# Performance work log

Measured on AMD Instinct MI355X. Metric: run time of the kernel, lower is better.

## Reference

```python
import jax, jax.numpy as jnp
import numpy as np

# --- fixed model configuration (from init_kwargs) ---
Nx, Nu, Ny, Np = 3, 1, 2, 5
Nz = Np * (Ny + Nu)          # 15
F, V, DELTA = 0.1, 1.0, 1.0  # ps (flow), volume, sampling time
CAMEAN, CBMEAN = 0.5, 0.4    # yscale means
CASTD, CBSTD = 0.3, 0.2      # yscale stds
CAFMEAN, CAFSTD = 1.0, 0.5   # uscale


def _fnn(x, W1, b1, W2, b2):
    # dense(tanh) -> dense(linear), as createDenseLayers/fnnTf
    return jnp.tanh(x @ W1 + b1) @ W2 + b2


def setup_inputs() -> dict:
    B, T = 4096, 1024
    key = jax.random.key(0)
    ks = jax.random.split(key, 16)
    g = lambda k, shp, fan: (jax.random.normal(k, shp, jnp.float32) / np.sqrt(fan))
    return {
        "u": jax.random.normal(ks[0], (B, T, Nu), jnp.float32),
        "xz0": jax.random.normal(ks[1], (B, Nx + Nz), jnp.float32),
        "r1_W1": g(ks[2], (1, 16), 1),  "r1_b1": jnp.zeros((16,), jnp.float32),
        "r1_W2": g(ks[3], (16, 1), 16), "r1_b2": jnp.zeros((1,), jnp.float32),
        "r2_W1": g(ks[4], (2, 16), 2),  "r2_b1": jnp.zeros((16,), jnp.float32),
        "r2_W2": g(ks[5], (16, 1), 16), "r2_b2": jnp.zeros((1,), jnp.float32),
        "eC_W1": g(ks[6], (Nz, 32), Nz), "eC_b1": jnp.zeros((32,), jnp.float32),
        "eC_W2": g(ks[7], (32, 1), 32),  "eC_b2": jnp.zeros((1,), jnp.float32),
    }


def _forward(u, xz0, r1_W1, r1_b1, r1_W2, r1_b2,
             r2_W1, r2_b1, r2_W2, r2_b2, eC_W1, eC_b1, eC_W2, eC_b2):

    def fxu(x, uu):
        Ca, Cb, Cc = x[:, 0:1], x[:, 1:2], x[:, 2:3]
        Caf = uu[:, 0:1]
        r1 = _fnn(Ca, r1_W1, r1_b1, r1_W2, r1_b2) * CASTD
        r2 = _fnn(jnp.concatenate((Cb, Cc), -1), r2_W1, r2_b1, r2_W2, r2_b2) * CBSTD
        Ca = Ca * CASTD + CAMEAN
        Cb = Cb * CBSTD + CBMEAN
        Cc = Cc * CBSTD + CBMEAN
        Caf = Caf * CAFSTD + CAFMEAN
        dCa = F * (Caf - Ca) / V - r1
        dCb = -F * Cb / V + r1 - 3.0 * r2
        dCc = -F * Cc / V + r2
        return jnp.concatenate([dCa / CASTD, dCb / CBSTD, dCc / CBSTD], -1)

    # initial state: replace Cc with NN estimate from past data z0
    y0 = xz0[:, :Ny]
    z0 = xz0[:, Nx:]
    Cc0 = _fnn(z0, eC_W1, eC_b1, eC_W2, eC_b2)
    xz = jnp.concatenate((y0, Cc0, z0), -1)  # [B, Nx+Nz]

    def step(xz, uu):
        x, z = xz[:, :Nx], xz[:, Nx:]
        ypseq, upseq = z[:, :Np * Ny], z[:, Np * Ny:]
        k1 = fxu(x, uu)
        k2 = fxu(x + DELTA * (k1 / 2.0), uu)
        k3 = fxu(x + DELTA * (k2 / 2.0), uu)
        k4 = fxu(x + DELTA * k3, uu)
        xplus = x + (DELTA / 6.0) * (k1 + 2.0 * k2 + 2.0 * k3 + k4)
        zplus = jnp.concatenate((ypseq[:, Ny:], x[:, :Ny], upseq[:, Nu:], uu), -1)
        CcNN = _fnn(z, eC_W1, eC_b1, eC_W2, eC_b2)
        y = jnp.concatenate((x, CcNN), -1)  # [B, Nx+1]
        return jnp.concatenate((xplus, zplus), -1), y

    u_t = jnp.swapaxes(u, 0, 1)  # [T, B, Nu]
    _, ys = jax.lax.scan(step, xz, u_t)
    yseq_full = jnp.swapaxes(ys, 0, 1)      # [B, T, Nx+1]
    yseq = yseq_full[..., :Ny]
    xseq = yseq_full[..., :Nx]
    return yseq_full, yseq, xseq


def reference(u, xz0, r1_W1, r1_b1, r1_W2, r1_b2,
              r2_W1, r2_b1, r2_W2, r2_b2, eC_W1, eC_b1, eC_W2, eC_b2):
    return _forward(u, xz0, r1_W1, r1_b1, r1_W2, r1_b2,
                    r2_W1, r2_b1, r2_W2, r2_b2, eC_W1, eC_b1, eC_W2, eC_b2)
```

## Files before the change

### kernel.cpp

```cpp
#include <hip/hip_runtime.h>
#include <stdint.h>
#include <math.h>

#define NB 4096
#define NT 1024


#if __has_builtin(__builtin_amdgcn_exp2f)
#define EXP2F __builtin_amdgcn_exp2f
#else
#define EXP2F exp2f
#endif
#if __has_builtin(__builtin_amdgcn_rcpf)
#define RCPF __builtin_amdgcn_rcpf
#else
#define RCPF(x) (1.0f / (x))
#endif

__device__ __forceinline__ float fast_tanh(float y) {
  float e = EXP2F(y * 2.885390081777927f);
  float r = RCPF(e + 1.0f);
  return __builtin_fmaf(-2.0f, r, 1.0f);
}

template <int CTRL>
__device__ __forceinline__ float dppmov(float x) {
  return __int_as_float(
      __builtin_amdgcn_update_dpp(0, __float_as_int(x), CTRL, 0xF, 0xF, true));
}

__device__ __forceinline__ void rowred2(float& a, float& b) {
  a += dppmov<0x128>(a); b += dppmov<0x128>(b);
  a += dppmov<0x124>(a); b += dppmov<0x124>(b);
  a += dppmov<0x122>(a); b += dppmov<0x122>(b);
  a += dppmov<0x121>(a); b += dppmov<0x121>(b);
}
__device__ __forceinline__ float rowred1(float a) {
  a += dppmov<0x128>(a);
  a += dppmov<0x124>(a);
  a += dppmov<0x122>(a);
  a += dppmov<0x121>(a);
  return a;
}

__global__ __launch_bounds__(256) void phase1_kernel(
    const float* __restrict__ u, const float* __restrict__ xz0,
    const float* __restrict__ r1W1, const float* __restrict__ r1b1,
    const float* __restrict__ r1W2, const float* __restrict__ r1b2,
    const float* __restrict__ r2W1, const float* __restrict__ r2b1,
    const float* __restrict__ r2W2, const float* __restrict__ r2b2,
    const float* __restrict__ eCW1, const float* __restrict__ eCb1,
    const float* __restrict__ eCW2, const float* __restrict__ eCb2,
    float* __restrict__ out) {
  const int lane = threadIdx.x & 15;
  const int chain = (blockIdx.x << 4) + (threadIdx.x >> 4);

  const float w1a = r1W1[lane];
  const float w1b = r1b1[lane];
  const float w1c = r1W2[lane];
  const float c1 = r1b2[0];
  const float w2a = r2W1[lane];
  const float w2b = r2W1[16 + lane];
  const float w2c = r2b1[lane];
  const float w2d = r2W2[lane];
  const float c2 = r2b2[0];

  const float* xzr = xz0 + chain * 18;
  float x0 = xzr[0];
  float x1 = xzr[1];

  float hA = eCb1[lane], hB = eCb1[lane + 16];
#pragma unroll
  for (int i = 0; i < 15; ++i) {
    const float z = xzr[3 + i];
    hA = __builtin_fmaf(z, eCW1[i * 32 + lane], hA);
    hB = __builtin_fmaf(z, eCW1[i * 32 + lane + 16], hB);
  }
  float p = fast_tanh(hA) * eCW2[lane] + fast_tanh(hB) * eCW2[lane + 16];
  float x2 = rowred1(p) + eCb2[0];

  const float* urow = u + (size_t)chain * NT;
  float* yf = out + (size_t)chain * NT * 4;
  float* ys = out + (size_t)NB * NT * 4 + (size_t)chain * NT * 2;
  float* xs = out + (size_t)NB * NT * 6 + (size_t)chain * NT * 3;

  float a_u;
  auto fxu = [&](float s0, float s1, float s2, float& k0, float& k1,
                 float& k2) {
    float p1 = fast_tanh(__builtin_fmaf(s0, w1a, w1b)) * w1c;
    float p2 =
        fast_tanh(__builtin_fmaf(s1, w2a, __builtin_fmaf(s2, w2b, w2c))) * w2d;
    rowred2(p1, p2);
    const float n1 = p1 + c1;
    const float n2 = p2 + c2;
    k0 = __builtin_fmaf(-0.1f, s0, a_u) - n1;
    float t1 = __builtin_fmaf(-0.1f, s1, -0.2f);
    t1 = __builtin_fmaf(1.5f, n1, t1);
    k1 = __builtin_fmaf(-3.0f, n2, t1);
    k2 = __builtin_fmaf(-0.1f, s2, -0.2f) + n2;
  };

  float4 ucur = *(const float4*)urow;
  for (int t4 = 0; t4 < NT; t4 += 4) {
    const int tn = (t4 + 4 < NT) ? (t4 + 4) : (NT - 4);
    const float4 unext = *(const float4*)(urow + tn);
    float us[4] = {ucur.x, ucur.y, ucur.z, ucur.w};
#pragma unroll
    for (int e = 0; e < 4; ++e) {
      const int t = t4 + e;
      if (lane == 0) {
        *(float2*)(yf + t * 4) = make_float2(x0, x1);
        yf[t * 4 + 2] = x2;
        *(float2*)(ys + t * 2) = make_float2(x0, x1);
        xs[t * 3 + 0] = x0;
        xs[t * 3 + 1] = x1;
        xs[t * 3 + 2] = x2;
      }
      const float uu = us[e];
      a_u = __builtin_fmaf(uu, 1.0f / 6.0f, 1.0f / 6.0f);
      float k10, k11, k12, k20, k21, k22, k30, k31, k32, k40, k41, k42;
      fxu(x0, x1, x2, k10, k11, k12);
      fxu(__builtin_fmaf(0.5f, k10, x0), __builtin_fmaf(0.5f, k11, x1),
          __builtin_fmaf(0.5f, k12, x2), k20, k21, k22);
      fxu(__builtin_fmaf(0.5f, k20, x0), __builtin_fmaf(0.5f, k21, x1),
          __builtin_fmaf(0.5f, k22, x2), k30, k31, k32);
      fxu(x0 + k30, x1 + k31, x2 + k32, k40, k41, k42);
      x0 += (k10 + 2.0f * (k20 + k30) + k40) * (1.0f / 6.0f);
      x1 += (k11 + 2.0f * (k21 + k31) + k41) * (1.0f / 6.0f);
      x2 += (k12 + 2.0f * (k22 + k32) + k42) * (1.0f / 6.0f);
    }
    ucur = unext;
  }
}

__global__ __launch_bounds__(256) void phase2_kernel(
    const float* __restrict__ u, const float* __restrict__ xz0,
    const float* __restrict__ eCW1, const float* __restrict__ eCb1,
    const float* __restrict__ eCW2, const float* __restrict__ eCb2,
    float* __restrict__ out) {
  __shared__ float lw[32][16];
  __shared__ float lw2[32];
  const int tid = threadIdx.x;
  if (tid < 32) {
#pragma unroll
    for (int i = 0; i < 15; ++i) lw[tid][i] = eCW1[i * 32 + tid];
    lw[tid][15] = eCb1[tid];
    lw2[tid] = eCW2[tid];
  }
  __syncthreads();

  const int b = blockIdx.x;
  const int t0 = tid << 2;
  const float2* ysrow =
      (const float2*)(out + (size_t)NB * NT * 4) + (size_t)b * NT;
  const float* urow = u + (size_t)b * NT;
  const float* xzr = xz0 + b * 18;

  float yw[16], uw[8];
#pragma unroll
  for (int idx = 0; idx < 8; ++idx) {
    const int tp = t0 - 5 + idx;
    float a, c, uu;
    if (tp >= 0) {
      const float2 h = ysrow[tp];
      a = h.x;
      c = h.y;
      uu = urow[tp];
    } else {
      a = xzr[3 + 2 * (tp + 5)];
      c = xzr[4 + 2 * (tp + 5)];
      uu = xzr[13 + (tp + 5)];
    }
    yw[2 * idx] = a;
    yw[2 * idx + 1] = c;
    uw[idx] = uu;
  }

  float acc[4] = {0.f, 0.f, 0.f, 0.f};
  for (int j = 0; j < 32; ++j) {
    const float4 wa = ((const float4*)lw[j])[0];
    const float4 wb = ((const float4*)lw[j])[1];
    const float4 wc = ((const float4*)lw[j])[2];
    const float4 wd = ((const float4*)lw[j])[3];
    const float w2 = lw2[j];
#pragma unroll
    for (int e = 0; e < 4; ++e) {
      float h = wd.w;
      h = __builtin_fmaf(yw[2 * e + 0], wa.x, h);
      h = __builtin_fmaf(yw[2 * e + 1], wa.y, h);
      h = __builtin_fmaf(yw[2 * e + 2], wa.z, h);
      h = __builtin_fmaf(yw[2 * e + 3], wa.w, h);
      h = __builtin_fmaf(yw[2 * e + 4], wb.x, h);
      h = __builtin_fmaf(yw[2 * e + 5], wb.y, h);
      h = __builtin_fmaf(yw[2 * e + 6], wb.z, h);
      h = __builtin_fmaf(yw[2 * e + 7], wb.w, h);
      h = __builtin_fmaf(yw[2 * e + 8], wc.x, h);
      h = __builtin_fmaf(yw[2 * e + 9], wc.y, h);
      h = __builtin_fmaf(uw[e + 0], wc.z, h);
      h = __builtin_fmaf(uw[e + 1], wc.w, h);
      h = __builtin_fmaf(uw[e + 2], wd.x, h);
      h = __builtin_fmaf(uw[e + 3], wd.y, h);
      h = __builtin_fmaf(uw[e + 4], wd.z, h);
      acc[e] = __builtin_fmaf(fast_tanh(h), w2, acc[e]);
    }
  }
  const float b2v = eCb2[0];
  float* yfrow = out + (size_t)b * NT * 4;
#pragma unroll
  for (int e = 0; e < 4; ++e) {
    yfrow[(t0 + e) * 4 + 3] = acc[e] + b2v;
  }
}

extern "C" void kernel_launch(void* const* d_in, const int* in_sizes, int n_in,
                              void* d_out, int out_size, void* d_ws,
                              size_t ws_size, hipStream_t stream) {
  const float* u = (const float*)d_in[0];
  const float* xz0 = (const float*)d_in[1];
  const float* r1W1 = (const float*)d_in[2];
  const float* r1b1 = (const float*)d_in[3];
  const float* r1W2 = (const float*)d_in[4];
  const float* r1b2 = (const float*)d_in[5];
  const float* r2W1 = (const float*)d_in[6];
  const float* r2b1 = (const float*)d_in[7];
  const float* r2W2 = (const float*)d_in[8];
  const float* r2b2 = (const float*)d_in[9];
  const float* eCW1 = (const float*)d_in[10];
  const float* eCb1 = (const float*)d_in[11];
  const float* eCW2 = (const float*)d_in[12];
  const float* eCb2 = (const float*)d_in[13];
  float* out = (float*)d_out;

  hipLaunchKernelGGL(phase1_kernel, dim3(NB / 16), dim3(256), 0, stream, u,
                     xz0, r1W1, r1b1, r1W2, r1b2, r2W1, r2b1, r2W2, r2b2, eCW1,
                     eCb1, eCW2, eCb2, out);
  hipLaunchKernelGGL(phase2_kernel, dim3(NB), dim3(256), 0, stream, u, xz0,
                     eCW1, eCb1, eCW2, eCb2, out);
}
```

Measured before the change: 680.6 us.

## Split RK4 state across two 16-lane DPP rows per chain and fold tanh constants

Phase 1 now gives each chain 32 lanes. One DPP row evaluates the r1 network and owns Ca, and the other row evaluates r2 and owns (Cb, Cc), so each lane computes a single tanh per RK stage instead of two. The r1 sum is broadcast across rows with a row_bcast DPP. The tanh scale and the -2*W2 factor are folded into the weights in both kernels, which removes multiplies from the inner loops. This doubles the thread count for phase 1 and lowers the work per lane on the serial recurrence, but it adds a cross-row DPP dependency and leaves more lanes idle during stores.

```diff
diff --git a/kernel.cpp b/kernel.cpp
--- a/kernel.cpp
+++ b/kernel.cpp
@@ -17,30 +17,29 @@
 #define RCPF(x) (1.0f / (x))
 #endif
 
-__device__ __forceinline__ float fast_tanh(float y) {
-  float e = EXP2F(y * 2.885390081777927f);
-  float r = RCPF(e + 1.0f);
-  return __builtin_fmaf(-2.0f, r, 1.0f);
-}
+#define TANH_SCALE 2.885390081777927f
 
 template <int CTRL>
 __device__ __forceinline__ float dppmov(float x) {
   return __int_as_float(
       __builtin_amdgcn_update_dpp(0, __float_as_int(x), CTRL, 0xF, 0xF, true));
 }
-
-__device__ __forceinline__ void rowred2(float& a, float& b) {
-  a += dppmov<0x128>(a); b += dppmov<0x128>(b);
-  a += dppmov<0x124>(a); b += dppmov<0x124>(b);
-  a += dppmov<0x122>(a); b += dppmov<0x122>(b);
-  a += dppmov<0x121>(a); b += dppmov<0x121>(b);
-}
+template <int CTRL, int RMASK>
+__device__ __forceinline__ float dppmov_keep(float x) {
+  return __int_as_float(__builtin_amdgcn_update_dpp(
+      __float_as_int(x), __float_as_int(x), CTRL, RMASK, 0xF, false));
+}
+
 __device__ __forceinline__ float rowred1(float a) {
   a += dppmov<0x128>(a);
   a += dppmov<0x124>(a);
   a += dppmov<0x122>(a);
   a += dppmov<0x121>(a);
   return a;
+}
+
+__device__ __forceinline__ float bcast_r1sum(float x) {
+  return dppmov_keep<0x142, 0xA>(x);
 }
 
 __global__ __launch_bounds__(256) void phase1_kernel(
@@ -52,82 +51,105 @@
     const float* __restrict__ eCW1, const float* __restrict__ eCb1,
     const float* __restrict__ eCW2, const float* __restrict__ eCb2,
     float* __restrict__ out) {
-  const int lane = threadIdx.x & 15;
-  const int chain = (blockIdx.x << 4) + (threadIdx.x >> 4);
-
-  const float w1a = r1W1[lane];
-  const float w1b = r1b1[lane];
-  const float w1c = r1W2[lane];
+  const int tid = threadIdx.x;
+  const int sub = tid & 31;
+  const int rl = tid & 15;
+  const bool row1 = (sub & 16) != 0;
+  const int chain = (blockIdx.x << 3) + (tid >> 5);
+
+  float wA, wB, wC, wP;
+  if (!row1) {
+    wA = r1W1[rl] * TANH_SCALE;
+    wB = 0.0f;
+    wC = r1b1[rl] * TANH_SCALE;
+    wP = r1W2[rl];
+  } else {
+    wA = r2W1[rl] * TANH_SCALE;
+    wB = r2W1[16 + rl] * TANH_SCALE;
+    wC = r2b1[rl] * TANH_SCALE;
+    wP = r2W2[rl];
+  }
+  const float wPn2 = -2.0f * wP;
   const float c1 = r1b2[0];
-  const float w2a = r2W1[lane];
-  const float w2b = r2W1[16 + lane];
-  const float w2c = r2b1[lane];
-  const float w2d = r2W2[lane];
   const float c2 = r2b2[0];
 
+  const float gA1 = row1 ? 1.5f : -1.0f;
+  const float gA2 = row1 ? -3.0f : 0.0f;
+  const float mB = row1 ? -0.1f : 0.0f;
+  const float cBc = row1 ? -0.2f : 0.0f;
+  const float gB2 = row1 ? 1.0f : 0.0f;
+  const float uCoef = row1 ? 0.0f : (1.0f / 6.0f);
+  const float uBias = row1 ? -0.2f : (1.0f / 6.0f);
+
   const float* xzr = xz0 + chain * 18;
-  float x0 = xzr[0];
-  float x1 = xzr[1];
-
-  float hA = eCb1[lane], hB = eCb1[lane + 16];
-#pragma unroll
-  for (int i = 0; i < 15; ++i) {
-    const float z = xzr[3 + i];
-    hA = __builtin_fmaf(z, eCW1[i * 32 + lane], hA);
-    hB = __builtin_fmaf(z, eCW1[i * 32 + lane + 16], hB);
-  }
-  float p = fast_tanh(hA) * eCW2[lane] + fast_tanh(hB) * eCW2[lane + 16];
-  float x2 = rowred1(p) + eCb2[0];
+  float xA = row1 ? xzr[1] : xzr[0];
+
+  float h0 = eCb1[sub];
+#pragma unroll
+  for (int i = 0; i < 15; ++i)
+    h0 = __builtin_fmaf(xzr[3 + i], eCW1[i * 32 + sub], h0);
+  const float e0 = EXP2F(h0 * TANH_SCALE);
+  const float r0 = RCPF(e0 + 1.0f);
+  float p0 = __builtin_fmaf(-2.0f * eCW2[sub], r0, eCW2[sub]);
+  p0 = rowred1(p0);
+  const float q0 = __int_as_float(
+      __builtin_amdgcn_ds_swizzle(__float_as_int(p0), 0x401F));
+  const float x2init = p0 + q0 + eCb2[0];
+  float xB = row1 ? x2init : 0.0f;
 
   const float* urow = u + (size_t)chain * NT;
-  float* yf = out + (size_t)chain * NT * 4;
-  float* ys = out + (size_t)NB * NT * 4 + (size_t)chain * NT * 2;
-  float* xs = out + (size_t)NB * NT * 6 + (size_t)chain * NT * 3;
-
-  float a_u;
-  auto fxu = [&](float s0, float s1, float s2, float& k0, float& k1,
-                 float& k2) {
-    float p1 = fast_tanh(__builtin_fmaf(s0, w1a, w1b)) * w1c;
-    float p2 =
-        fast_tanh(__builtin_fmaf(s1, w2a, __builtin_fmaf(s2, w2b, w2c))) * w2d;
-    rowred2(p1, p2);
-    const float n1 = p1 + c1;
-    const float n2 = p2 + c2;
-    k0 = __builtin_fmaf(-0.1f, s0, a_u) - n1;
-    float t1 = __builtin_fmaf(-0.1f, s1, -0.2f);
-    t1 = __builtin_fmaf(1.5f, n1, t1);
-    k1 = __builtin_fmaf(-3.0f, n2, t1);
-    k2 = __builtin_fmaf(-0.1f, s2, -0.2f) + n2;
+  const int ro = row1 ? 1 : 0;
+  float* yfb = out + (size_t)chain * NT * 4 + ro;
+  float* ysb = out + (size_t)NB * NT * 4 + (size_t)chain * NT * 2 + ro;
+  float* xsb = out + (size_t)NB * NT * 6 + (size_t)chain * NT * 3 + ro;
+
+  auto fxu = [&](float sA, float sB, float cA, float& kA, float& kB) {
+    float h = __builtin_fmaf(sB, wB, wC);
+    h = __builtin_fmaf(sA, wA, h);
+    const float e = EXP2F(h);
+    const float r = RCPF(e + 1.0f);
+    float p = __builtin_fmaf(wPn2, r, wP);
+    p = rowred1(p);
+    const float n1 = bcast_r1sum(p) + c1;
+    const float n2 = p + c2;
+    kA = __builtin_fmaf(-0.1f, sA, cA);
+    kA = __builtin_fmaf(gA1, n1, kA);
+    kA = __builtin_fmaf(gA2, n2, kA);
+    kB = __builtin_fmaf(mB, sB, cBc);
+    kB = __builtin_fmaf(gB2, n2, kB);
   };
 
   float4 ucur = *(const float4*)urow;
   for (int t4 = 0; t4 < NT; t4 += 4) {
     const int tn = (t4 + 4 < NT) ? (t4 + 4) : (NT - 4);
     const float4 unext = *(const float4*)(urow + tn);
-    float us[4] = {ucur.x, ucur.y, ucur.z, ucur.w};
+    const float us[4] = {ucur.x, ucur.y, ucur.z, ucur.w};
 #pragma unroll
     for (int e = 0; e < 4; ++e) {
       const int t = t4 + e;
-      if (lane == 0) {
-        *(float2*)(yf + t * 4) = make_float2(x0, x1);
-        yf[t * 4 + 2] = x2;
-        *(float2*)(ys + t * 2) = make_float2(x0, x1);
-        xs[t * 3 + 0] = x0;
-        xs[t * 3 + 1] = x1;
-        xs[t * 3 + 2] = x2;
+      if (rl == 0) {
+        yfb[t * 4] = xA;
+        ysb[t * 2] = xA;
+        xsb[t * 3] = xA;
       }
-      const float uu = us[e];
-      a_u = __builtin_fmaf(uu, 1.0f / 6.0f, 1.0f / 6.0f);
-      float k10, k11, k12, k20, k21, k22, k30, k31, k32, k40, k41, k42;
-      fxu(x0, x1, x2, k10, k11, k12);
-      fxu(__builtin_fmaf(0.5f, k10, x0), __builtin_fmaf(0.5f, k11, x1),
-          __builtin_fmaf(0.5f, k12, x2), k20, k21, k22);
-      fxu(__builtin_fmaf(0.5f, k20, x0), __builtin_fmaf(0.5f, k21, x1),
-          __builtin_fmaf(0.5f, k22, x2), k30, k31, k32);
-      fxu(x0 + k30, x1 + k31, x2 + k32, k40, k41, k42);
-      x0 += (k10 + 2.0f * (k20 + k30) + k40) * (1.0f / 6.0f);
-      x1 += (k11 + 2.0f * (k21 + k31) + k41) * (1.0f / 6.0f);
-      x2 += (k12 + 2.0f * (k22 + k32) + k42) * (1.0f / 6.0f);
+      if (sub == 16) {
+        yfb[t * 4 + 1] = xB;
+        xsb[t * 3 + 1] = xB;
+      }
+      const float cA = __builtin_fmaf(us[e], uCoef, uBias);
+      float k1A, k1B, k2A, k2B, k3A, k3B, k4A, k4B;
+      fxu(xA, xB, cA, k1A, k1B);
+      fxu(__builtin_fmaf(0.5f, k1A, xA), __builtin_fmaf(0.5f, k1B, xB), cA,
+          k2A, k2B);
+      fxu(__builtin_fmaf(0.5f, k2A, xA), __builtin_fmaf(0.5f, k2B, xB), cA,
+          k3A, k3B);
+      fxu(xA + k3A, xB + k3B, cA, k4A, k4B);
+      float tA = k2A + k3A;
+      tA = __builtin_fmaf(2.0f, tA, k1A) + k4A;
+      xA = __builtin_fmaf(1.0f / 6.0f, tA, xA);
+      float tB = k2B + k3B;
+      tB = __builtin_fmaf(2.0f, tB, k1B) + k4B;
+      xB = __builtin_fmaf(1.0f / 6.0f, tB, xB);
     }
     ucur = unext;
   }
@@ -143,9 +165,9 @@
   const int tid = threadIdx.x;
   if (tid < 32) {
 #pragma unroll
-    for (int i = 0; i < 15; ++i) lw[tid][i] = eCW1[i * 32 + tid];
-    lw[tid][15] = eCb1[tid];
-    lw2[tid] = eCW2[tid];
+    for (int i = 0; i < 15; ++i) lw[tid][i] = eCW1[i * 32 + tid] * TANH_SCALE;
+    lw[tid][15] = eCb1[tid] * TANH_SCALE;
+    lw2[tid] = -2.0f * eCW2[tid];
   }
   __syncthreads();
 
@@ -182,7 +204,7 @@
     const float4 wb = ((const float4*)lw[j])[1];
     const float4 wc = ((const float4*)lw[j])[2];
     const float4 wd = ((const float4*)lw[j])[3];
-    const float w2 = lw2[j];
+    const float w2n = lw2[j];
 #pragma unroll
     for (int e = 0; e < 4; ++e) {
       float h = wd.w;
@@ -201,14 +223,18 @@
       h = __builtin_fmaf(uw[e + 2], wd.x, h);
       h = __builtin_fmaf(uw[e + 3], wd.y, h);
       h = __builtin_fmaf(uw[e + 4], wd.z, h);
-      acc[e] = __builtin_fmaf(fast_tanh(h), w2, acc[e]);
+      const float r = RCPF(EXP2F(h) + 1.0f);
+      acc[e] = __builtin_fmaf(w2n, r, acc[e]);
     }
   }
-  const float b2v = eCb2[0];
+  float sw = 0.0f;
+#pragma unroll
+  for (int j = 0; j < 32; ++j) sw += eCW2[j];
+  const float C = eCb2[0] + sw;
   float* yfrow = out + (size_t)b * NT * 4;
 #pragma unroll
   for (int e = 0; e < 4; ++e) {
-    yfrow[(t0 + e) * 4 + 3] = acc[e] + b2v;
+    yfrow[(t0 + e) * 4 + 3] = acc[e] + C;
   }
 }
 
@@ -231,8 +257,8 @@
   const float* eCb2 = (const float*)d_in[13];
   float* out = (float*)d_out;
 
-  hipLaunchKernelGGL(phase1_kernel, dim3(NB / 16), dim3(256), 0, stream, u,
-                     xz0, r1W1, r1b1, r1W2, r1b2, r2W1, r2b1, r2W2, r2b2, eCW1,
+  hipLaunchKernelGGL(phase1_kernel, dim3(NB / 8), dim3(256), 0, stream, u, xz0,
+                     r1W1, r1b1, r1W2, r1b2, r2W1, r2b1, r2W2, r2b2, eCW1,
                      eCb1, eCW2, eCb2, out);
   hipLaunchKernelGGL(phase2_kernel, dim3(NB), dim3(256), 0, stream, u, xz0,
                      eCW1, eCb1, eCW2, eCb2, out);
```

Measured after the change: 682.8 us. No clear change (+0.3%).

## Fuse Cc estimator into recurrence kernel and spread output stores across lanes

Applied to the files above, without the earlier changes.

Merges the two-kernel approach into one kernel: the eC network for each timestep is computed inline within the 16-lane group, using a sliding register window of past y and u instead of a second kernel that re-reads the stored y sequence. Output writes are spread across lanes (each lane owns one output column) rather than funnelled through lane 0. Tanh scaling constants and biases are folded into the weights so each activation needs fewer ops. Blocks shrink to 64 threads. This adds about 32 extra FMAs plus 2 exp/rcp and one reduction per step to the serial critical path, traded against removing the second kernel launch and its memory traffic.

```diff
diff --git a/kernel.cpp b/kernel.cpp
--- a/kernel.cpp
+++ b/kernel.cpp
@@ -17,11 +17,7 @@
 #define RCPF(x) (1.0f / (x))
 #endif
 
-__device__ __forceinline__ float fast_tanh(float y) {
-  float e = EXP2F(y * 2.885390081777927f);
-  float r = RCPF(e + 1.0f);
-  return __builtin_fmaf(-2.0f, r, 1.0f);
-}
+#define TS 2.885390081777927f
 
 template <int CTRL>
 __device__ __forceinline__ float dppmov(float x) {
@@ -43,7 +39,7 @@
   return a;
 }
 
-__global__ __launch_bounds__(256) void phase1_kernel(
+__global__ __launch_bounds__(64) void fused_kernel(
     const float* __restrict__ u, const float* __restrict__ xz0,
     const float* __restrict__ r1W1, const float* __restrict__ r1b1,
     const float* __restrict__ r1W2, const float* __restrict__ r1b2,
@@ -52,163 +48,152 @@
     const float* __restrict__ eCW1, const float* __restrict__ eCb1,
     const float* __restrict__ eCW2, const float* __restrict__ eCb2,
     float* __restrict__ out) {
-  const int lane = threadIdx.x & 15;
-  const int chain = (blockIdx.x << 4) + (threadIdx.x >> 4);
-
-  const float w1a = r1W1[lane];
-  const float w1b = r1b1[lane];
-  const float w1c = r1W2[lane];
+  const int tid = threadIdx.x;
+  const int cl = tid & 15;
+  const int chain = (blockIdx.x << 2) + (tid >> 4);
+
+  const float wA1 = r1W1[cl] * TS;
+  const float wC1 = r1b1[cl] * TS;
+  const float wP1 = r1W2[cl];
+  const float wP1n2 = -2.0f * wP1;
+  const float wA2 = r2W1[cl] * TS;
+  const float wB2 = r2W1[16 + cl] * TS;
+  const float wC2 = r2b1[cl] * TS;
+  const float wP2 = r2W2[cl];
+  const float wP2n2 = -2.0f * wP2;
   const float c1 = r1b2[0];
-  const float w2a = r2W1[lane];
-  const float w2b = r2W1[16 + lane];
-  const float w2c = r2b1[lane];
-  const float w2d = r2W2[lane];
   const float c2 = r2b2[0];
+  const float C0b = 1.0f / 6.0f - c1;
+  const float C1 = -0.2f + 1.5f * c1 - 3.0f * c2;
+  const float C2 = c2 - 0.2f;
+
+  float eWa[15], eWb[15];
+#pragma unroll
+  for (int i = 0; i < 15; ++i) {
+    eWa[i] = eCW1[i * 32 + cl] * TS;
+    eWb[i] = eCW1[i * 32 + cl + 16] * TS;
+  }
+  const float ebA = eCb1[cl] * TS;
+  const float ebB = eCb1[cl + 16] * TS;
+  const float ew2a = eCW2[cl];
+  const float ew2b = eCW2[cl + 16];
+  const float ew2an2 = -2.0f * ew2a;
+  const float ew2bn2 = -2.0f * ew2b;
+  const float ew2sum = ew2a + ew2b;
+  const float eb2v = eCb2[0];
 
   const float* xzr = xz0 + chain * 18;
   float x0 = xzr[0];
   float x1 = xzr[1];
 
-  float hA = eCb1[lane], hB = eCb1[lane + 16];
-#pragma unroll
-  for (int i = 0; i < 15; ++i) {
-    const float z = xzr[3 + i];
-    hA = __builtin_fmaf(z, eCW1[i * 32 + lane], hA);
-    hB = __builtin_fmaf(z, eCW1[i * 32 + lane + 16], hB);
+  float zy[10], zu[5];
+#pragma unroll
+  for (int i = 0; i < 10; ++i) zy[i] = xzr[3 + i];
+#pragma unroll
+  for (int i = 0; i < 5; ++i) zu[i] = xzr[13 + i];
+
+  auto eC = [&]() -> float {
+    float ha = ebA, hb = ebB;
+#pragma unroll
+    for (int i = 0; i < 10; ++i) {
+      ha = __builtin_fmaf(zy[i], eWa[i], ha);
+      hb = __builtin_fmaf(zy[i], eWb[i], hb);
+    }
+#pragma unroll
+    for (int i = 0; i < 5; ++i) {
+      ha = __builtin_fmaf(zu[i], eWa[10 + i], ha);
+      hb = __builtin_fmaf(zu[i], eWb[10 + i], hb);
+    }
+    const float ra = RCPF(EXP2F(ha) + 1.0f);
+    const float rb = RCPF(EXP2F(hb) + 1.0f);
+    float pl = __builtin_fmaf(ew2an2, ra, ew2sum);
+    pl = __builtin_fmaf(ew2bn2, rb, pl);
+    pl = rowred1(pl);
+    return pl + eb2v;
+  };
+
+  float x2 = eC();
+
+  const int clp = (cl < 9) ? cl : (cl - 7);
+  size_t idx0;
+  int stride;
+  if (clp < 4) {
+    idx0 = (size_t)chain * NT * 4 + clp;
+    stride = 4;
+  } else if (clp < 6) {
+    idx0 = (size_t)NB * NT * 4 + (size_t)chain * NT * 2 + (clp - 4);
+    stride = 2;
+  } else {
+    idx0 = (size_t)NB * NT * 6 + (size_t)chain * NT * 3 + (clp - 6);
+    stride = 3;
   }
-  float p = fast_tanh(hA) * eCW2[lane] + fast_tanh(hB) * eCW2[lane + 16];
-  float x2 = rowred1(p) + eCb2[0];
+  float* sp = out + idx0;
+  const bool selx0 = (clp == 0) || (clp == 4) || (clp == 6);
+  const bool selx1 = (clp == 1) || (clp == 5) || (clp == 7);
+  const bool selCc = (clp == 3);
+
+  float C0t;
+  auto stage = [&](float s0, float s1, float s2, float& k0, float& k1,
+                   float& k2) {
+    const float u0 = __builtin_fmaf(-0.1f, s0, C0t);
+    const float u1 = __builtin_fmaf(-0.1f, s1, C1);
+    const float u2 = __builtin_fmaf(-0.1f, s2, C2);
+    const float hA = __builtin_fmaf(s0, wA1, wC1);
+    const float hB =
+        __builtin_fmaf(s1, wA2, __builtin_fmaf(s2, wB2, wC2));
+    const float rA = RCPF(EXP2F(hA) + 1.0f);
+    const float rB = RCPF(EXP2F(hB) + 1.0f);
+    float pA = __builtin_fmaf(wP1n2, rA, wP1);
+    float pB = __builtin_fmaf(wP2n2, rB, wP2);
+    rowred2(pA, pB);
+    k0 = u0 - pA;
+    k1 = __builtin_fmaf(-3.0f, pB, __builtin_fmaf(1.5f, pA, u1));
+    k2 = u2 + pB;
+  };
 
   const float* urow = u + (size_t)chain * NT;
-  float* yf = out + (size_t)chain * NT * 4;
-  float* ys = out + (size_t)NB * NT * 4 + (size_t)chain * NT * 2;
-  float* xs = out + (size_t)NB * NT * 6 + (size_t)chain * NT * 3;
-
-  float a_u;
-  auto fxu = [&](float s0, float s1, float s2, float& k0, float& k1,
-                 float& k2) {
-    float p1 = fast_tanh(__builtin_fmaf(s0, w1a, w1b)) * w1c;
-    float p2 =
-        fast_tanh(__builtin_fmaf(s1, w2a, __builtin_fmaf(s2, w2b, w2c))) * w2d;
-    rowred2(p1, p2);
-    const float n1 = p1 + c1;
-    const float n2 = p2 + c2;
-    k0 = __builtin_fmaf(-0.1f, s0, a_u) - n1;
-    float t1 = __builtin_fmaf(-0.1f, s1, -0.2f);
-    t1 = __builtin_fmaf(1.5f, n1, t1);
-    k1 = __builtin_fmaf(-3.0f, n2, t1);
-    k2 = __builtin_fmaf(-0.1f, s2, -0.2f) + n2;
-  };
-
   float4 ucur = *(const float4*)urow;
   for (int t4 = 0; t4 < NT; t4 += 4) {
     const int tn = (t4 + 4 < NT) ? (t4 + 4) : (NT - 4);
     const float4 unext = *(const float4*)(urow + tn);
-    float us[4] = {ucur.x, ucur.y, ucur.z, ucur.w};
+    const float us4[4] = {ucur.x, ucur.y, ucur.z, ucur.w};
 #pragma unroll
     for (int e = 0; e < 4; ++e) {
-      const int t = t4 + e;
-      if (lane == 0) {
-        *(float2*)(yf + t * 4) = make_float2(x0, x1);
-        yf[t * 4 + 2] = x2;
-        *(float2*)(ys + t * 2) = make_float2(x0, x1);
-        xs[t * 3 + 0] = x0;
-        xs[t * 3 + 1] = x1;
-        xs[t * 3 + 2] = x2;
-      }
-      const float uu = us[e];
-      a_u = __builtin_fmaf(uu, 1.0f / 6.0f, 1.0f / 6.0f);
-      float k10, k11, k12, k20, k21, k22, k30, k31, k32, k40, k41, k42;
-      fxu(x0, x1, x2, k10, k11, k12);
-      fxu(__builtin_fmaf(0.5f, k10, x0), __builtin_fmaf(0.5f, k11, x1),
-          __builtin_fmaf(0.5f, k12, x2), k20, k21, k22);
-      fxu(__builtin_fmaf(0.5f, k20, x0), __builtin_fmaf(0.5f, k21, x1),
-          __builtin_fmaf(0.5f, k22, x2), k30, k31, k32);
-      fxu(x0 + k30, x1 + k31, x2 + k32, k40, k41, k42);
-      x0 += (k10 + 2.0f * (k20 + k30) + k40) * (1.0f / 6.0f);
-      x1 += (k11 + 2.0f * (k21 + k31) + k41) * (1.0f / 6.0f);
-      x2 += (k12 + 2.0f * (k22 + k32) + k42) * (1.0f / 6.0f);
+      const float uu = us4[e];
+      const float Cc = eC();
+      const float v = selx0 ? x0 : (selx1 ? x1 : (selCc ? Cc : x2));
+      *sp = v;
+      sp += stride;
+#pragma unroll
+      for (int i = 0; i < 8; ++i) zy[i] = zy[i + 2];
+      zy[8] = x0;
+      zy[9] = x1;
+#pragma unroll
+      for (int i = 0; i < 4; ++i) zu[i] = zu[i + 1];
+      zu[4] = uu;
+      C0t = __builtin_fmaf(uu, 1.0f / 6.0f, C0b);
+      float p0, p1, p2, q0, q1, q2;
+      stage(x0, x1, x2, p0, p1, p2);
+      float a0 = p0, a1 = p1, a2 = p2;
+      stage(__builtin_fmaf(0.5f, p0, x0), __builtin_fmaf(0.5f, p1, x1),
+            __builtin_fmaf(0.5f, p2, x2), q0, q1, q2);
+      a0 = __builtin_fmaf(2.0f, q0, a0);
+      a1 = __builtin_fmaf(2.0f, q1, a1);
+      a2 = __builtin_fmaf(2.0f, q2, a2);
+      stage(__builtin_fmaf(0.5f, q0, x0), __builtin_fmaf(0.5f, q1, x1),
+            __builtin_fmaf(0.5f, q2, x2), p0, p1, p2);
+      a0 = __builtin_fmaf(2.0f, p0, a0);
+      a1 = __builtin_fmaf(2.0f, p1, a1);
+      a2 = __builtin_fmaf(2.0f, p2, a2);
+      stage(x0 + p0, x1 + p1, x2 + p2, q0, q1, q2);
+      a0 += q0;
+      a1 += q1;
+      a2 += q2;
+      x0 = __builtin_fmaf(1.0f / 6.0f, a0, x0);
+      x1 = __builtin_fmaf(1.0f / 6.0f, a1, x1);
+      x2 = __builtin_fmaf(1.0f / 6.0f, a2, x2);
     }
     ucur = unext;
-  }
-}
-
-__global__ __launch_bounds__(256) void phase2_kernel(
-    const float* __restrict__ u, const float* __restrict__ xz0,
-    const float* __restrict__ eCW1, const float* __restrict__ eCb1,
-    const float* __restrict__ eCW2, const float* __restrict__ eCb2,
-    float* __restrict__ out) {
-  __shared__ float lw[32][16];
-  __shared__ float lw2[32];
-  const int tid = threadIdx.x;
-  if (tid < 32) {
-#pragma unroll
-    for (int i = 0; i < 15; ++i) lw[tid][i] = eCW1[i * 32 + tid];
-    lw[tid][15] = eCb1[tid];
-    lw2[tid] = eCW2[tid];
-  }
-  __syncthreads();
-
-  const int b = blockIdx.x;
-  const int t0 = tid << 2;
-  const float2* ysrow =
-      (const float2*)(out + (size_t)NB * NT * 4) + (size_t)b * NT;
-  const float* urow = u + (size_t)b * NT;
-  const float* xzr = xz0 + b * 18;
-
-  float yw[16], uw[8];
-#pragma unroll
-  for (int idx = 0; idx < 8; ++idx) {
-    const int tp = t0 - 5 + idx;
-    float a, c, uu;
-    if (tp >= 0) {
-      const float2 h = ysrow[tp];
-      a = h.x;
-      c = h.y;
-      uu = urow[tp];
-    } else {
-      a = xzr[3 + 2 * (tp + 5)];
-      c = xzr[4 + 2 * (tp + 5)];
-      uu = xzr[13 + (tp + 5)];
-    }
-    yw[2 * idx] = a;
-    yw[2 * idx + 1] = c;
-    uw[idx] = uu;
-  }
-
-  float acc[4] = {0.f, 0.f, 0.f, 0.f};
-  for (int j = 0; j < 32; ++j) {
-    const float4 wa = ((const float4*)lw[j])[0];
-    const float4 wb = ((const float4*)lw[j])[1];
-    const float4 wc = ((const float4*)lw[j])[2];
-    const float4 wd = ((const float4*)lw[j])[3];
-    const float w2 = lw2[j];
-#pragma unroll
-    for (int e = 0; e < 4; ++e) {
-      float h = wd.w;
-      h = __builtin_fmaf(yw[2 * e + 0], wa.x, h);
-      h = __builtin_fmaf(yw[2 * e + 1], wa.y, h);
-      h = __builtin_fmaf(yw[2 * e + 2], wa.z, h);
-      h = __builtin_fmaf(yw[2 * e + 3], wa.w, h);
-      h = __builtin_fmaf(yw[2 * e + 4], wb.x, h);
-      h = __builtin_fmaf(yw[2 * e + 5], wb.y, h);
-      h = __builtin_fmaf(yw[2 * e + 6], wb.z, h);
-      h = __builtin_fmaf(yw[2 * e + 7], wb.w, h);
-      h = __builtin_fmaf(yw[2 * e + 8], wc.x, h);
-      h = __builtin_fmaf(yw[2 * e + 9], wc.y, h);
-      h = __builtin_fmaf(uw[e + 0], wc.z, h);
-      h = __builtin_fmaf(uw[e + 1], wc.w, h);
-      h = __builtin_fmaf(uw[e + 2], wd.x, h);
-      h = __builtin_fmaf(uw[e + 3], wd.y, h);
-      h = __builtin_fmaf(uw[e + 4], wd.z, h);
-      acc[e] = __builtin_fmaf(fast_tanh(h), w2, acc[e]);
-    }
-  }
-  const float b2v = eCb2[0];
-  float* yfrow = out + (size_t)b * NT * 4;
-#pragma unroll
-  for (int e = 0; e < 4; ++e) {
-    yfrow[(t0 + e) * 4 + 3] = acc[e] + b2v;
   }
 }
 
@@ -231,9 +216,7 @@
   const float* eCb2 = (const float*)d_in[13];
   float* out = (float*)d_out;
 
-  hipLaunchKernelGGL(phase1_kernel, dim3(NB / 16), dim3(256), 0, stream, u,
-                     xz0, r1W1, r1b1, r1W2, r1b2, r2W1, r2b1, r2W2, r2b2, eCW1,
+  hipLaunchKernelGGL(fused_kernel, dim3(NB / 4), dim3(64), 0, stream, u, xz0,
+                     r1W1, r1b1, r1W2, r1b2, r2W1, r2b1, r2W2, r2b2, eCW1,
                      eCb1, eCW2, eCb2, out);
-  hipLaunchKernelGGL(phase2_kernel, dim3(NB), dim3(256), 0, stream, u, xz0,
-                     eCW1, eCb1, eCW2, eCb2, out);
-}
+}
```

Result: slower. 742.7 us (+9.1%).

## Fold tanh scaling into weights, propagate RK4 hidden pre-activations, spread stores

Applied to the files above, without the earlier changes.

Pre-scales the MLP weights by the exp2 constant and folds the tanh affine term into the output weights and bias, so each tanh becomes exp2 plus a reciprocal plus one FMA. RK4 stage pre-activations are now formed incrementally from the base pre-activation plus a scaled k term, and the constant terms of the derivative are merged into precomputed offsets. Output stores are spread across lanes (each lane writes one output component with its own stride) instead of lane 0 doing all seven writes. Blocks shrink to 64 threads with more blocks. The rearranged arithmetic could change rounding slightly.

```diff
diff --git a/kernel.cpp b/kernel.cpp
--- a/kernel.cpp
+++ b/kernel.cpp
@@ -17,11 +17,7 @@
 #define RCPF(x) (1.0f / (x))
 #endif
 
-__device__ __forceinline__ float fast_tanh(float y) {
-  float e = EXP2F(y * 2.885390081777927f);
-  float r = RCPF(e + 1.0f);
-  return __builtin_fmaf(-2.0f, r, 1.0f);
-}
+#define TS 2.885390081777927f
 
 template <int CTRL>
 __device__ __forceinline__ float dppmov(float x) {
@@ -43,7 +39,7 @@
   return a;
 }
 
-__global__ __launch_bounds__(256) void phase1_kernel(
+__global__ __launch_bounds__(64) void phase1_kernel(
     const float* __restrict__ u, const float* __restrict__ xz0,
     const float* __restrict__ r1W1, const float* __restrict__ r1b1,
     const float* __restrict__ r1W2, const float* __restrict__ r1b2,
@@ -52,82 +48,130 @@
     const float* __restrict__ eCW1, const float* __restrict__ eCb1,
     const float* __restrict__ eCW2, const float* __restrict__ eCb2,
     float* __restrict__ out) {
-  const int lane = threadIdx.x & 15;
-  const int chain = (blockIdx.x << 4) + (threadIdx.x >> 4);
-
-  const float w1a = r1W1[lane];
-  const float w1b = r1b1[lane];
-  const float w1c = r1W2[lane];
+  const int tid = threadIdx.x;
+  const int cl = tid & 15;
+  const int chain = (blockIdx.x << 2) + (tid >> 4);
+
+  const float wA1 = r1W1[cl] * TS;
+  const float wC1 = r1b1[cl] * TS;
+  const float wP1 = r1W2[cl];
+  const float wP1n2 = -2.0f * wP1;
+  const float wA2 = r2W1[cl] * TS;
+  const float wB2 = r2W1[16 + cl] * TS;
+  const float wC2 = r2b1[cl] * TS;
+  const float wP2 = r2W2[cl];
+  const float wP2n2 = -2.0f * wP2;
+  const float wA1h = 0.5f * wA1;
+  const float wA2h = 0.5f * wA2;
+  const float wB2h = 0.5f * wB2;
   const float c1 = r1b2[0];
-  const float w2a = r2W1[lane];
-  const float w2b = r2W1[16 + lane];
-  const float w2c = r2b1[lane];
-  const float w2d = r2W2[lane];
   const float c2 = r2b2[0];
+  const float C0b = 1.0f / 6.0f - c1;
+  const float C1 = -0.2f + 1.5f * c1 - 3.0f * c2;
+  const float C2 = c2 - 0.2f;
 
   const float* xzr = xz0 + chain * 18;
   float x0 = xzr[0];
   float x1 = xzr[1];
-
-  float hA = eCb1[lane], hB = eCb1[lane + 16];
-#pragma unroll
-  for (int i = 0; i < 15; ++i) {
-    const float z = xzr[3 + i];
-    hA = __builtin_fmaf(z, eCW1[i * 32 + lane], hA);
-    hB = __builtin_fmaf(z, eCW1[i * 32 + lane + 16], hB);
-  }
-  float p = fast_tanh(hA) * eCW2[lane] + fast_tanh(hB) * eCW2[lane + 16];
-  float x2 = rowred1(p) + eCb2[0];
+  float x2;
+
+  {
+    float ha = eCb1[cl] * TS, hb = eCb1[cl + 16] * TS;
+#pragma unroll
+    for (int i = 0; i < 15; ++i) {
+      const float z = xzr[3 + i];
+      ha = __builtin_fmaf(z, eCW1[i * 32 + cl] * TS, ha);
+      hb = __builtin_fmaf(z, eCW1[i * 32 + cl + 16] * TS, hb);
+    }
+    const float w2a = eCW2[cl], w2b = eCW2[cl + 16];
+    const float ra = RCPF(EXP2F(ha) + 1.0f);
+    const float rb = RCPF(EXP2F(hb) + 1.0f);
+    float pl = __builtin_fmaf(-2.0f * w2a, ra, w2a + w2b);
+    pl = __builtin_fmaf(-2.0f * w2b, rb, pl);
+    pl = rowred1(pl);
+    x2 = pl + eCb2[0];
+  }
+
+  const int clp = (cl < 8) ? cl : (cl - 8);
+  size_t idx0;
+  int stride;
+  if (clp < 3) {
+    idx0 = (size_t)chain * NT * 4 + clp;
+    stride = 4;
+  } else if (clp < 5) {
+    idx0 = (size_t)NB * NT * 4 + (size_t)chain * NT * 2 + (clp - 3);
+    stride = 2;
+  } else {
+    idx0 = (size_t)NB * NT * 6 + (size_t)chain * NT * 3 + (clp - 5);
+    stride = 3;
+  }
+  float* sp = out + idx0;
+  const bool selx0 = (clp == 0) || (clp == 3) || (clp == 5);
+  const bool selx1 = (clp == 1) || (clp == 4) || (clp == 6);
+
+  auto nets = [&](float hA, float hB, float& S1, float& S2) {
+    const float rA = RCPF(EXP2F(hA) + 1.0f);
+    const float rB = RCPF(EXP2F(hB) + 1.0f);
+    float pA = __builtin_fmaf(wP1n2, rA, wP1);
+    float pB = __builtin_fmaf(wP2n2, rB, wP2);
+    rowred2(pA, pB);
+    S1 = pA;
+    S2 = pB;
+  };
 
   const float* urow = u + (size_t)chain * NT;
-  float* yf = out + (size_t)chain * NT * 4;
-  float* ys = out + (size_t)NB * NT * 4 + (size_t)chain * NT * 2;
-  float* xs = out + (size_t)NB * NT * 6 + (size_t)chain * NT * 3;
-
-  float a_u;
-  auto fxu = [&](float s0, float s1, float s2, float& k0, float& k1,
-                 float& k2) {
-    float p1 = fast_tanh(__builtin_fmaf(s0, w1a, w1b)) * w1c;
-    float p2 =
-        fast_tanh(__builtin_fmaf(s1, w2a, __builtin_fmaf(s2, w2b, w2c))) * w2d;
-    rowred2(p1, p2);
-    const float n1 = p1 + c1;
-    const float n2 = p2 + c2;
-    k0 = __builtin_fmaf(-0.1f, s0, a_u) - n1;
-    float t1 = __builtin_fmaf(-0.1f, s1, -0.2f);
-    t1 = __builtin_fmaf(1.5f, n1, t1);
-    k1 = __builtin_fmaf(-3.0f, n2, t1);
-    k2 = __builtin_fmaf(-0.1f, s2, -0.2f) + n2;
-  };
-
   float4 ucur = *(const float4*)urow;
   for (int t4 = 0; t4 < NT; t4 += 4) {
     const int tn = (t4 + 4 < NT) ? (t4 + 4) : (NT - 4);
     const float4 unext = *(const float4*)(urow + tn);
-    float us[4] = {ucur.x, ucur.y, ucur.z, ucur.w};
+    const float us4[4] = {ucur.x, ucur.y, ucur.z, ucur.w};
 #pragma unroll
     for (int e = 0; e < 4; ++e) {
-      const int t = t4 + e;
-      if (lane == 0) {
-        *(float2*)(yf + t * 4) = make_float2(x0, x1);
-        yf[t * 4 + 2] = x2;
-        *(float2*)(ys + t * 2) = make_float2(x0, x1);
-        xs[t * 3 + 0] = x0;
-        xs[t * 3 + 1] = x1;
-        xs[t * 3 + 2] = x2;
-      }
-      const float uu = us[e];
-      a_u = __builtin_fmaf(uu, 1.0f / 6.0f, 1.0f / 6.0f);
-      float k10, k11, k12, k20, k21, k22, k30, k31, k32, k40, k41, k42;
-      fxu(x0, x1, x2, k10, k11, k12);
-      fxu(__builtin_fmaf(0.5f, k10, x0), __builtin_fmaf(0.5f, k11, x1),
-          __builtin_fmaf(0.5f, k12, x2), k20, k21, k22);
-      fxu(__builtin_fmaf(0.5f, k20, x0), __builtin_fmaf(0.5f, k21, x1),
-          __builtin_fmaf(0.5f, k22, x2), k30, k31, k32);
-      fxu(x0 + k30, x1 + k31, x2 + k32, k40, k41, k42);
-      x0 += (k10 + 2.0f * (k20 + k30) + k40) * (1.0f / 6.0f);
-      x1 += (k11 + 2.0f * (k21 + k31) + k41) * (1.0f / 6.0f);
-      x2 += (k12 + 2.0f * (k22 + k32) + k42) * (1.0f / 6.0f);
+      const float v = selx0 ? x0 : (selx1 ? x1 : x2);
+      *sp = v;
+      sp += stride;
+      const float C0t = __builtin_fmaf(us4[e], 1.0f / 6.0f, C0b);
+      const float u0x = __builtin_fmaf(-0.1f, x0, C0t);
+      const float u1x = __builtin_fmaf(-0.1f, x1, C1);
+      const float u2x = __builtin_fmaf(-0.1f, x2, C2);
+      const float hAx = __builtin_fmaf(x0, wA1, wC1);
+      const float hBx = __builtin_fmaf(x1, wA2, __builtin_fmaf(x2, wB2, wC2));
+      float S1, S2;
+      nets(hAx, hBx, S1, S2);
+      const float k10 = u0x - S1;
+      const float k11 =
+          __builtin_fmaf(1.5f, S1, __builtin_fmaf(-3.0f, S2, u1x));
+      const float k12 = u2x + S2;
+      nets(__builtin_fmaf(wA1h, k10, hAx),
+           __builtin_fmaf(wA2h, k11, __builtin_fmaf(wB2h, k12, hBx)), S1, S2);
+      const float k20 = __builtin_fmaf(-0.05f, k10, u0x) - S1;
+      const float k21 = __builtin_fmaf(
+          1.5f, S1,
+          __builtin_fmaf(-3.0f, S2, __builtin_fmaf(-0.05f, k11, u1x)));
+      const float k22 = __builtin_fmaf(-0.05f, k12, u2x) + S2;
+      nets(__builtin_fmaf(wA1h, k20, hAx),
+           __builtin_fmaf(wA2h, k21, __builtin_fmaf(wB2h, k22, hBx)), S1, S2);
+      const float k30 = __builtin_fmaf(-0.05f, k20, u0x) - S1;
+      const float k31 = __builtin_fmaf(
+          1.5f, S1,
+          __builtin_fmaf(-3.0f, S2, __builtin_fmaf(-0.05f, k21, u1x)));
+      const float k32 = __builtin_fmaf(-0.05f, k22, u2x) + S2;
+      nets(__builtin_fmaf(wA1, k30, hAx),
+           __builtin_fmaf(wA2, k31, __builtin_fmaf(wB2, k32, hBx)), S1, S2);
+      const float k40 = __builtin_fmaf(-0.1f, k30, u0x) - S1;
+      const float k41 = __builtin_fmaf(
+          1.5f, S1,
+          __builtin_fmaf(-3.0f, S2, __builtin_fmaf(-0.1f, k31, u1x)));
+      const float k42 = __builtin_fmaf(-0.1f, k32, u2x) + S2;
+      float a0 = k20 + k30;
+      a0 = __builtin_fmaf(2.0f, a0, k10) + k40;
+      x0 = __builtin_fmaf(1.0f / 6.0f, a0, x0);
+      float a1 = k21 + k31;
+      a1 = __builtin_fmaf(2.0f, a1, k11) + k41;
+      x1 = __builtin_fmaf(1.0f / 6.0f, a1, x1);
+      float a2 = k22 + k32;
+      a2 = __builtin_fmaf(2.0f, a2, k12) + k42;
+      x2 = __builtin_fmaf(1.0f / 6.0f, a2, x2);
     }
     ucur = unext;
   }
@@ -143,9 +187,9 @@
   const int tid = threadIdx.x;
   if (tid < 32) {
 #pragma unroll
-    for (int i = 0; i < 15; ++i) lw[tid][i] = eCW1[i * 32 + tid];
-    lw[tid][15] = eCb1[tid];
-    lw2[tid] = eCW2[tid];
+    for (int i = 0; i < 15; ++i) lw[tid][i] = eCW1[i * 32 + tid] * TS;
+    lw[tid][15] = eCb1[tid] * TS;
+    lw2[tid] = -2.0f * eCW2[tid];
   }
   __syncthreads();
 
@@ -182,7 +226,7 @@
     const float4 wb = ((const float4*)lw[j])[1];
     const float4 wc = ((const float4*)lw[j])[2];
     const float4 wd = ((const float4*)lw[j])[3];
-    const float w2 = lw2[j];
+    const float w2n = lw2[j];
 #pragma unroll
     for (int e = 0; e < 4; ++e) {
       float h = wd.w;
@@ -201,14 +245,18 @@
       h = __builtin_fmaf(uw[e + 2], wd.x, h);
       h = __builtin_fmaf(uw[e + 3], wd.y, h);
       h = __builtin_fmaf(uw[e + 4], wd.z, h);
-      acc[e] = __builtin_fmaf(fast_tanh(h), w2, acc[e]);
-    }
-  }
-  const float b2v = eCb2[0];
+      const float r = RCPF(EXP2F(h) + 1.0f);
+      acc[e] = __builtin_fmaf(w2n, r, acc[e]);
+    }
+  }
+  float sw = 0.0f;
+#pragma unroll
+  for (int j = 0; j < 32; ++j) sw += eCW2[j];
+  const float C = eCb2[0] + sw;
   float* yfrow = out + (size_t)b * NT * 4;
 #pragma unroll
   for (int e = 0; e < 4; ++e) {
-    yfrow[(t0 + e) * 4 + 3] = acc[e] + b2v;
+    yfrow[(t0 + e) * 4 + 3] = acc[e] + C;
   }
 }
 
@@ -231,8 +279,8 @@
   const float* eCb2 = (const float*)d_in[13];
   float* out = (float*)d_out;
 
-  hipLaunchKernelGGL(phase1_kernel, dim3(NB / 16), dim3(256), 0, stream, u,
-                     xz0, r1W1, r1b1, r1W2, r1b2, r2W1, r2b1, r2W2, r2b2, eCW1,
+  hipLaunchKernelGGL(phase1_kernel, dim3(NB / 4), dim3(64), 0, stream, u, xz0,
+                     r1W1, r1b1, r1W2, r1b2, r2W1, r2b1, r2W2, r2b2, eCW1,
                      eCb1, eCW2, eCb2, out);
   hipLaunchKernelGGL(phase2_kernel, dim3(NB), dim3(256), 0, stream, u, xz0,
                      eCW1, eCb1, eCW2, eCb2, out);
```

New measurement: 685.7 us. No clear change (+0.7%).
